# Optimization experiments

Measured on AMD Instinct MI355X. Metric: run time of the kernel, lower is better.

The kernel has to match this reference:

```python
import jax, jax.numpy as jnp
import numpy as np

LEAK = 0.01
EPS = 1e-5


def _gcn(x, W, b, src, dst, n):
    # GCNConv: add self-loops, symmetric D^-1/2 (A+I) D^-1/2 normalization
    h = x @ W
    loop = jnp.arange(n)
    s = jnp.concatenate([src, loop])
    d = jnp.concatenate([dst, loop])
    deg = jax.ops.segment_sum(jnp.ones(s.shape[0], h.dtype), d, num_segments=n)
    dinv = jnp.where(deg > 0, jax.lax.rsqrt(deg), 0.0)
    norm = dinv[s] * dinv[d]
    out = jax.ops.segment_sum(h[s] * norm[:, None], d, num_segments=n)
    return out + b


def _sage(x, Wl, bl, Wr, src, dst, n):
    # SAGEConv (mean aggr): lin_l(mean_neigh) + lin_r(x); bias on lin_l
    cnt = jax.ops.segment_sum(jnp.ones(src.shape[0], x.dtype), dst, num_segments=n)
    agg = jax.ops.segment_sum(x[src], dst, num_segments=n) / jnp.maximum(cnt, 1.0)[:, None]
    return agg @ Wl + bl + x @ Wr


def _bn(x, g, b):
    # BatchNorm over node dim, batch statistics (training forward), biased var
    m = x.mean(0)
    v = jnp.mean((x - m) ** 2, axis=0)
    return (x - m) * jax.lax.rsqrt(v + EPS) * g + b


def _lrelu(x):
    return jnp.where(x >= 0, x, LEAK * x)


def setup_inputs() -> dict:
    key = jax.random.key(0)
    ks = jax.random.split(key, 20)
    N, E, F_IN, H, G, L = 50000, 800000, 128, 128, 1000, 1000
    h2, h4, OUT = H // 2, H // 4, 32
    x = jax.random.normal(ks[0], (N, F_IN), dtype=jnp.float32)
    edge_index = jax.random.randint(ks[1], (2, E), 0, N)
    batch = jnp.sort(jax.random.randint(ks[2], (N,), 0, G))
    link_indices = jax.random.randint(ks[3], (2, L), 0, G)
    s = 0.05
    return {
        "x": x, "edge_index": edge_index, "batch": batch,
        "link_indices": link_indices, "num_graphs": G,
        "W1": jax.random.normal(ks[4], (F_IN, H), jnp.float32) * s,
        "b1": jnp.zeros((H,), jnp.float32),
        "g1": jnp.ones((H,), jnp.float32), "be1": jnp.zeros((H,), jnp.float32),
        "Wl2": jax.random.normal(ks[5], (H, h2), jnp.float32) * s,
        "bl2": jnp.zeros((h2,), jnp.float32),
        "Wr2": jax.random.normal(ks[6], (H, h2), jnp.float32) * s,
        "g2": jnp.ones((h2,), jnp.float32), "be2": jnp.zeros((h2,), jnp.float32),
        "W3": jax.random.normal(ks[7], (h2, h4), jnp.float32) * s,
        "b3": jnp.zeros((h4,), jnp.float32),
        "g3": jnp.ones((h4,), jnp.float32), "be3": jnp.zeros((h4,), jnp.float32),
        "W4": jax.random.normal(ks[8], (h4, OUT), jnp.float32) * s,
        "b4": jnp.zeros((OUT,), jnp.float32),
    }


def reference(x, edge_index, batch, link_indices, num_graphs,
              W1, b1, g1, be1, Wl2, bl2, Wr2, g2, be2,
              W3, b3, g3, be3, W4, b4):
    n = x.shape[0]
    src, dst = edge_index[0], edge_index[1]
    h = _lrelu(_bn(_gcn(x, W1, b1, src, dst, n), g1, be1))        # dropout = identity (eval)
    h = _lrelu(_bn(_sage(h, Wl2, bl2, Wr2, src, dst, n), g2, be2))
    h = _lrelu(_bn(_gcn(h, W3, b3, src, dst, n), g3, be3))
    h = _gcn(h, W4, b4, src, dst, n)
    g = jax.ops.segment_sum(h, batch, num_segments=num_graphs)     # global_add_pool
    src_emb = g[link_indices[0]]
    tgt_emb = g[link_indices[1]]
    return jax.nn.sigmoid(jnp.sum(src_emb * tgt_emb, axis=1))
```

## Files before the change

kernel.cpp:

```cpp
#include <hip/hip_runtime.h>
#include <math.h>

#define LEAK 0.01f
#define BNEPS 1e-5f
#define NCH 256
#define NGMAX 1024

__device__ inline unsigned bfpack(float a, float b) {
  unsigned ua = __float_as_uint(a);
  unsigned ub = __float_as_uint(b);
  unsigned ra = (ua + 0x7fffu + ((ua >> 16) & 1u)) >> 16;
  unsigned rb = (ub + 0x7fffu + ((ub >> 16) & 1u)) & 0xffff0000u;
  return ra | rb;
}
__device__ inline float2 bfunpack(unsigned u) {
  float2 r;
  r.x = __uint_as_float(u << 16);
  r.y = __uint_as_float(u & 0xffff0000u);
  return r;
}

__global__ __launch_bounds__(256) void k_hist(const int* __restrict__ dst,
                                              int* __restrict__ H, int E, int NBK) {
  __shared__ int h[256];
  h[threadIdx.x] = 0;
  __syncthreads();
  int chunk = (E + NCH - 1) / NCH;
  int lo = blockIdx.x * chunk, hi = min(lo + chunk, E);
  for (int e = lo + threadIdx.x; e < hi; e += 256)
    atomicAdd(&h[dst[e] >> 8], 1);
  __syncthreads();
  if (threadIdx.x < NBK) H[threadIdx.x * NCH + blockIdx.x] = h[threadIdx.x];
}

__global__ __launch_bounds__(256) void k_gscan1(const int* __restrict__ in,
                                                int* __restrict__ bsum, int m) {
  int i = blockIdx.x * 256 + threadIdx.x;
  int v = (i < m) ? in[i] : 0;
#pragma unroll
  for (int s = 1; s < 64; s <<= 1) v += __shfl_xor(v, s, 64);
  __shared__ int ws[4];
  if ((threadIdx.x & 63) == 0) ws[threadIdx.x >> 6] = v;
  __syncthreads();
  if (threadIdx.x == 0) bsum[blockIdx.x] = ws[0] + ws[1] + ws[2] + ws[3];
}
__global__ __launch_bounds__(256) void k_gscan2(int* __restrict__ bsum, int NB) {
  __shared__ int lds[256];
  int t = threadIdx.x;
  int v = (t < NB) ? bsum[t] : 0;
  lds[t] = v;
  __syncthreads();
  for (int ofs = 1; ofs < 256; ofs <<= 1) {
    int u = (t >= ofs) ? lds[t - ofs] : 0;
    __syncthreads();
    lds[t] += u;
    __syncthreads();
  }
  if (t < NB) bsum[t] = lds[t] - v;
}
__global__ __launch_bounds__(256) void k_gscan3(const int* __restrict__ in,
                                                const int* __restrict__ boff,
                                                int* __restrict__ out, int m) {
  __shared__ int lds[256];
  int t = threadIdx.x;
  int i = blockIdx.x * 256 + t;
  int v = (i < m) ? in[i] : 0;
  lds[t] = v;
  __syncthreads();
  for (int ofs = 1; ofs < 256; ofs <<= 1) {
    int u = (t >= ofs) ? lds[t - ofs] : 0;
    __syncthreads();
    lds[t] += u;
    __syncthreads();
  }
  if (i < m) out[i] = boff[blockIdx.x] + lds[t] - v;
}

__global__ __launch_bounds__(256) void k_scatter_bkt(
    const int* __restrict__ src, const int* __restrict__ dst,
    const int* __restrict__ O, int* __restrict__ ebuf, int E, int NBK) {
  __shared__ int cur[256];
  if (threadIdx.x < NBK) cur[threadIdx.x] = O[threadIdx.x * NCH + blockIdx.x];
  __syncthreads();
  int chunk = (E + NCH - 1) / NCH;
  int lo = blockIdx.x * chunk, hi = min(lo + chunk, E);
  for (int e = lo + threadIdx.x; e < hi; e += 256) {
    int d = dst[e];
    int pos = atomicAdd(&cur[d >> 8], 1);
    ebuf[pos] = src[e] | ((d & 255) << 24);
  }
}

__global__ __launch_bounds__(256) void k_fill2(
    const int* __restrict__ ebuf, const int* __restrict__ O,
    int* __restrict__ eidx, int* __restrict__ rowptr,
    float* __restrict__ dinv, float* __restrict__ invcnt,
    int E, int n, int NBK) {
  __shared__ int hist[256];
  __shared__ int sc[256];
  __shared__ int cur[256];
  const int b = blockIdx.x;
  const int t = threadIdx.x;
  const int lo = O[b * NCH];
  const int hi = (b + 1 < NBK) ? O[(b + 1) * NCH] : E;
  hist[t] = 0;
  __syncthreads();
  for (int e = lo + t; e < hi; e += 256)
    atomicAdd(&hist[(ebuf[e] >> 24) & 255], 1);
  __syncthreads();
  int v = hist[t];
  sc[t] = v;
  __syncthreads();
  for (int ofs = 1; ofs < 256; ofs <<= 1) {
    int u = (t >= ofs) ? sc[t - ofs] : 0;
    __syncthreads();
    sc[t] += u;
    __syncthreads();
  }
  int excl = sc[t] - v;
  cur[t] = lo + excl;
  int node = b * 256 + t;
  if (node < n) {
    rowptr[node] = lo + excl;
    float d = (float)v;
    dinv[node]   = rsqrtf(d + 1.0f);
    invcnt[node] = 1.0f / fmaxf(d, 1.0f);
  }
  if (node == n || (b == NBK - 1 && t == 255)) rowptr[n] = E;
  __syncthreads();
  for (int e = lo + t; e < hi; e += 256) {
    int p = ebuf[e];
    int pos = atomicAdd(&cur[(p >> 24) & 255], 1);
    eidx[pos] = p & 0xFFFFFF;
  }
}

template<int F, bool GCN, bool OUTBF, bool ADD>
__global__ __launch_bounds__(256) void k_gather(
    const unsigned short* __restrict__ Hs, const float* __restrict__ scale,
    const int* __restrict__ rowptr, const int* __restrict__ eidx,
    const float* __restrict__ bias, const float* __restrict__ addf,
    float* __restrict__ outf, unsigned short* __restrict__ outb, int n) {
  constexpr int COLS = F / 8;
  constexpr int EPI  = 64 / COLS;
  const int v = blockIdx.x * 4 + (threadIdx.x >> 6);
  if (v >= n) return;
  const int lane = threadIdx.x & 63;
  const int col  = lane % COLS;
  const int eo   = lane / COLS;

  const int lo = rowptr[v], hi = rowptr[v + 1];
  float a[8] = {0.f,0.f,0.f,0.f,0.f,0.f,0.f,0.f};
  int myE = (lo + lane < hi) ? eidx[lo + lane] : 0;
  for (int base = lo; base < hi; base += 64) {
    int cnt = min(hi - base, 64);
    int nxt = (base + 64 + lane < hi) ? eidx[base + 64 + lane] : 0;
#pragma unroll 4
    for (int t = eo; t < cnt; t += EPI) {
      int s = __shfl(myE, t, 64);
      uint4 hv = *(const uint4*)&Hs[(long long)s * F + col * 8];
      float2 p0 = bfunpack(hv.x), p1 = bfunpack(hv.y);
      float2 p2 = bfunpack(hv.z), p3 = bfunpack(hv.w);
      a[0]+=p0.x; a[1]+=p0.y; a[2]+=p1.x; a[3]+=p1.y;
      a[4]+=p2.x; a[5]+=p2.y; a[6]+=p3.x; a[7]+=p3.y;
    }
    myE = nxt;
  }
#pragma unroll
  for (int m = COLS; m < 64; m <<= 1) {
#pragma unroll
    for (int j = 0; j < 8; j++) a[j] += __shfl_xor(a[j], m, 64);
  }
  if (eo == 0) {
    float sv = scale[v];
    float o[8];
    if constexpr (GCN) {
      uint4 hv = *(const uint4*)&Hs[(long long)v * F + col * 8];
      float2 p0 = bfunpack(hv.x), p1 = bfunpack(hv.y);
      float2 p2 = bfunpack(hv.z), p3 = bfunpack(hv.w);
      float h[8] = {p0.x,p0.y,p1.x,p1.y,p2.x,p2.y,p3.x,p3.y};
#pragma unroll
      for (int j = 0; j < 8; j++) o[j] = bias[col * 8 + j] + sv * (a[j] + h[j]);
    } else if constexpr (ADD) {
      const float4 t0 = *(const float4*)&addf[(long long)v * F + col * 8];
      const float4 t1 = *(const float4*)&addf[(long long)v * F + col * 8 + 4];
      o[0]=fmaf(sv,a[0],t0.x); o[1]=fmaf(sv,a[1],t0.y);
      o[2]=fmaf(sv,a[2],t0.z); o[3]=fmaf(sv,a[3],t0.w);
      o[4]=fmaf(sv,a[4],t1.x); o[5]=fmaf(sv,a[5],t1.y);
      o[6]=fmaf(sv,a[6],t1.z); o[7]=fmaf(sv,a[7],t1.w);
    } else {
#pragma unroll
      for (int j = 0; j < 8; j++) o[j] = sv * a[j];
    }
    if constexpr (OUTBF) {
      uint4 u;
      u.x = bfpack(o[0], o[1]); u.y = bfpack(o[2], o[3]);
      u.z = bfpack(o[4], o[5]); u.w = bfpack(o[6], o[7]);
      *(uint4*)&outb[(long long)v * F + col * 8] = u;
    } else {
      float4 o0 = {o[0],o[1],o[2],o[3]}, o1 = {o[4],o[5],o[6],o[7]};
      *(float4*)&outf[(long long)v * F + col * 8]     = o0;
      *(float4*)&outf[(long long)v * F + col * 8 + 4] = o1;
    }
  }
}

template<int K, int FOUT, int KC, int R, bool X1BF, bool BNIN>
__global__ __launch_bounds__(256) void k_gemm(
    const void* __restrict__ X1v, const float* __restrict__ Wa,
    const float* __restrict__ bnstats, const float* __restrict__ prescale,
    unsigned short* __restrict__ Yb, int n) {
  constexpr int TPR  = FOUT / 4;
  constexpr int RGN  = 256 / TPR;
  constexpr int ROWS = RGN * R;
  __shared__ float sX1[ROWS * K];
  __shared__ float sWa[KC * FOUT];
  __shared__ float sbn[BNIN ? 2 * K : 1];

  if constexpr (BNIN) {
    for (int i = threadIdx.x; i < 2 * K; i += 256) sbn[i] = bnstats[i];
    __syncthreads();
  }
  const int row0 = blockIdx.x * ROWS;
  if constexpr (X1BF) {
    const unsigned short* X1 = (const unsigned short*)X1v;
    for (int i = threadIdx.x; i < ROWS * K / 8; i += 256) {
      int r = i / (K / 8), k8 = (i % (K / 8)) * 8;
      int gr = row0 + r;
      uint4 raw = {0,0,0,0};
      if (gr < n) raw = *(const uint4*)&X1[(long long)gr * K + k8];
      float2 p0 = bfunpack(raw.x), p1 = bfunpack(raw.y);
      float2 p2 = bfunpack(raw.z), p3 = bfunpack(raw.w);
      float y[8] = {p0.x,p0.y,p1.x,p1.y,p2.x,p2.y,p3.x,p3.y};
      if constexpr (BNIN) {
#pragma unroll
        for (int j = 0; j < 8; j++) {
          float t = fmaf(y[j], sbn[k8 + j], sbn[K + k8 + j]);
          y[j] = (t >= 0.f) ? t : LEAK * t;
        }
      }
      float4 lo = {y[0],y[1],y[2],y[3]}, hi = {y[4],y[5],y[6],y[7]};
      *(float4*)&sX1[r * K + k8]     = lo;
      *(float4*)&sX1[r * K + k8 + 4] = hi;
    }
  } else {
    const float* X1 = (const float*)X1v;
    for (int i = threadIdx.x; i < ROWS * K / 4; i += 256) {
      int r = i / (K / 4), k4 = (i % (K / 4)) * 4;
      int gr = row0 + r;
      float4 vv = {0,0,0,0};
      if (gr < n) vv = *(const float4*)&X1[(long long)gr * K + k4];
      *(float4*)&sX1[r * K + k4] = vv;
    }
  }

  const int cg = threadIdx.x % TPR;
  const int rg = threadIdx.x / TPR;
  const int jc = cg * 4;
  float4 acc[R];
#pragma unroll
  for (int i = 0; i < R; i++) acc[i] = {0.f,0.f,0.f,0.f};

  for (int k0 = 0; k0 < K; k0 += KC) {
    __syncthreads();
    for (int i = threadIdx.x; i < KC * FOUT / 4; i += 256) {
      int kk = i / (FOUT / 4), j4 = (i % (FOUT / 4)) * 4;
      *(float4*)&sWa[kk * FOUT + j4] = *(const float4*)&Wa[(long long)(k0 + kk) * FOUT + j4];
    }
    __syncthreads();
#pragma unroll 8
    for (int kk = 0; kk < KC; kk++) {
      const float4 w = *(const float4*)&sWa[kk * FOUT + jc];
#pragma unroll
      for (int i = 0; i < R; i++) {
        float xv = sX1[(rg * R + i) * K + k0 + kk];
        acc[i].x = fmaf(xv, w.x, acc[i].x); acc[i].y = fmaf(xv, w.y, acc[i].y);
        acc[i].z = fmaf(xv, w.z, acc[i].z); acc[i].w = fmaf(xv, w.w, acc[i].w);
      }
    }
  }
#pragma unroll
  for (int i = 0; i < R; i++) {
    int gr = row0 + rg * R + i;
    if (gr >= n) continue;
    float4 o = acc[i];
    float ps = prescale ? prescale[gr] : 1.0f;
    uint2 u;
    u.x = bfpack(o.x * ps, o.y * ps);
    u.y = bfpack(o.z * ps, o.w * ps);
    *(uint2*)&Yb[(long long)gr * FOUT + jc] = u;
  }
}

template<int R>
__global__ __launch_bounds__(256) void k_gemm_sage(
    const unsigned short* __restrict__ X, const float* __restrict__ Wl,
    const float* __restrict__ Wr, const float* __restrict__ bl,
    const float* __restrict__ bnstats,
    unsigned short* __restrict__ t1, float* __restrict__ t2, int n) {
  constexpr int K = 128, F = 64, KC = 64;
  constexpr int TPR = F / 4;
  constexpr int RGN = 256 / TPR;
  constexpr int ROWS = RGN * R;
  __shared__ float sX[ROWS * K];
  __shared__ float sWl[KC * F];
  __shared__ float sWr[KC * F];
  __shared__ float sbn[2 * K];

  for (int i = threadIdx.x; i < 2 * K; i += 256) sbn[i] = bnstats[i];
  __syncthreads();
  const int row0 = blockIdx.x * ROWS;
  for (int i = threadIdx.x; i < ROWS * K / 8; i += 256) {
    int r = i / (K / 8), k8 = (i % (K / 8)) * 8;
    int gr = row0 + r;
    uint4 raw = {0,0,0,0};
    if (gr < n) raw = *(const uint4*)&X[(long long)gr * K + k8];
    float2 p0 = bfunpack(raw.x), p1 = bfunpack(raw.y);
    float2 p2 = bfunpack(raw.z), p3 = bfunpack(raw.w);
    float y[8] = {p0.x,p0.y,p1.x,p1.y,p2.x,p2.y,p3.x,p3.y};
#pragma unroll
    for (int j = 0; j < 8; j++) {
      float t = fmaf(y[j], sbn[k8 + j], sbn[K + k8 + j]);
      y[j] = (t >= 0.f) ? t : LEAK * t;
    }
    float4 lo = {y[0],y[1],y[2],y[3]}, hi = {y[4],y[5],y[6],y[7]};
    *(float4*)&sX[r * K + k8]     = lo;
    *(float4*)&sX[r * K + k8 + 4] = hi;
  }

  const int cg = threadIdx.x % TPR;
  const int rg = threadIdx.x / TPR;
  const int jc = cg * 4;
  float4 a1[R], a2[R];
#pragma unroll
  for (int i = 0; i < R; i++) { a1[i] = {0,0,0,0}; a2[i] = {0,0,0,0}; }

  for (int k0 = 0; k0 < K; k0 += KC) {
    __syncthreads();
    for (int i = threadIdx.x; i < KC * F / 4; i += 256) {
      int kk = i / (F / 4), j4 = (i % (F / 4)) * 4;
      *(float4*)&sWl[kk * F + j4] = *(const float4*)&Wl[(long long)(k0 + kk) * F + j4];
      *(float4*)&sWr[kk * F + j4] = *(const float4*)&Wr[(long long)(k0 + kk) * F + j4];
    }
    __syncthreads();
#pragma unroll 8
    for (int kk = 0; kk < KC; kk++) {
      const float4 wl = *(const float4*)&sWl[kk * F + jc];
      const float4 wr = *(const float4*)&sWr[kk * F + jc];
#pragma unroll
      for (int i = 0; i < R; i++) {
        float xv = sX[(rg * R + i) * K + k0 + kk];
        a1[i].x = fmaf(xv, wl.x, a1[i].x); a1[i].y = fmaf(xv, wl.y, a1[i].y);
        a1[i].z = fmaf(xv, wl.z, a1[i].z); a1[i].w = fmaf(xv, wl.w, a1[i].w);
        a2[i].x = fmaf(xv, wr.x, a2[i].x); a2[i].y = fmaf(xv, wr.y, a2[i].y);
        a2[i].z = fmaf(xv, wr.z, a2[i].z); a2[i].w = fmaf(xv, wr.w, a2[i].w);
      }
    }
  }
#pragma unroll
  for (int i = 0; i < R; i++) {
    int gr = row0 + rg * R + i;
    if (gr >= n) continue;
    uint2 u;
    u.x = bfpack(a1[i].x, a1[i].y);
    u.y = bfpack(a1[i].z, a1[i].w);
    *(uint2*)&t1[(long long)gr * F + jc] = u;
    float4 o = a2[i];
    o.x += bl[jc]; o.y += bl[jc+1]; o.z += bl[jc+2]; o.w += bl[jc+3];
    *(float4*)&t2[(long long)gr * F + jc] = o;
  }
}

template<int F>
__global__ __launch_bounds__(256) void k_bn_stats(const unsigned short* __restrict__ Y,
                                                  float* __restrict__ partials, int n) {
  constexpr int FP  = F / 2;
  constexpr int RPB = 256 / FP;
  const int f2 = threadIdx.x % FP;
  const int r0 = threadIdx.x / FP;
  const unsigned* Yu = (const unsigned*)Y;
  float s1a = 0.f, s2a = 0.f, s1b = 0.f, s2b = 0.f;
  for (long long r = (long long)blockIdx.x * RPB + r0; r < n; r += 256LL * RPB) {
    float2 p = bfunpack(Yu[r * FP + f2]);
    s1a += p.x; s2a += p.x * p.x;
    s1b += p.y; s2b += p.y * p.y;
  }
  __shared__ float l1a[256], l2a[256], l1b[256], l2b[256];
  l1a[threadIdx.x] = s1a; l2a[threadIdx.x] = s2a;
  l1b[threadIdx.x] = s1b; l2b[threadIdx.x] = s2b;
  __syncthreads();
  if (r0 == 0) {
#pragma unroll
    for (int i = 1; i < RPB; i++) {
      s1a += l1a[i * FP + f2]; s2a += l2a[i * FP + f2];
      s1b += l1b[i * FP + f2]; s2b += l2b[i * FP + f2];
    }
    float* p = &partials[blockIdx.x * 2 * F];
    p[2 * f2]         = s1a;
    p[2 * f2 + 1]     = s1b;
    p[F + 2 * f2]     = s2a;
    p[F + 2 * f2 + 1] = s2b;
  }
}

__global__ void k_bn_finalize(const float* __restrict__ partials, float* __restrict__ stats,
                              const float* __restrict__ g, const float* __restrict__ be,
                              int F, float invN) {
  int f = threadIdx.x;
  if (f >= F) return;
  float s1 = 0.f, s2 = 0.f;
  for (int b = 0; b < 256; b++) {
    s1 += partials[b * 2 * F + f];
    s2 += partials[b * 2 * F + F + f];
  }
  float m   = s1 * invN;
  float var = s2 * invN - m * m;
  float sc  = g[f] * rsqrtf(var + BNEPS);
  stats[f]     = sc;
  stats[F + f] = be[f] - m * sc;
}

__global__ __launch_bounds__(256) void k_pool2(const float* __restrict__ a4,
                                               const int* __restrict__ batch,
                                               float* __restrict__ gpool, int n) {
  int g = blockIdx.x * 4 + (threadIdx.x >> 6);
  if (g >= NGMAX) return;
  int lane = threadIdx.x & 63;
  int s = 0, e = n;
  while (s < e) { int m = (s + e) >> 1; if (batch[m] < g) s = m + 1; else e = m; }
  int s2 = s, e2 = n;
  while (s2 < e2) { int m = (s2 + e2) >> 1; if (batch[m] < g + 1) s2 = m + 1; else e2 = m; }
  int f = lane & 31, ro = lane >> 5;
  float acc = 0.f;
  for (int r = s + ro; r < s2; r += 2) acc += a4[(long long)r * 32 + f];
  acc += __shfl_xor(acc, 32, 64);
  if (lane < 32) gpool[(long long)g * 32 + f] = acc;
}

__global__ void k_link(const float* __restrict__ g, const int* __restrict__ li0,
                       const int* __restrict__ li1, float* __restrict__ out, int L) {
  int i = blockIdx.x * blockDim.x + threadIdx.x;
  if (i >= L) return;
  const float* a = g + (long long)li0[i] * 32;
  const float* b = g + (long long)li1[i] * 32;
  float s = 0.f;
#pragma unroll
  for (int f = 0; f < 32; f++) s = fmaf(a[f], b[f], s);
  out[i] = 1.0f / (1.0f + expf(-s));
}

extern "C" void kernel_launch(void* const* d_in, const int* in_sizes, int n_in,
                              void* d_out, int out_size, void* d_ws, size_t ws_size,
                              hipStream_t stream) {
  const float* x   = (const float*)d_in[0];
  const int* ei    = (const int*)d_in[1];
  const int* batch = (const int*)d_in[2];
  const int* li    = (const int*)d_in[3];
  const float* W1  = (const float*)d_in[5];
  const float* b1  = (const float*)d_in[6];
  const float* g1  = (const float*)d_in[7];
  const float* be1 = (const float*)d_in[8];
  const float* Wl2 = (const float*)d_in[9];
  const float* bl2 = (const float*)d_in[10];
  const float* Wr2 = (const float*)d_in[11];
  const float* g2  = (const float*)d_in[12];
  const float* be2 = (const float*)d_in[13];
  const float* W3  = (const float*)d_in[14];
  const float* b3  = (const float*)d_in[15];
  const float* g3  = (const float*)d_in[16];
  const float* be3 = (const float*)d_in[17];
  const float* W4  = (const float*)d_in[18];
  const float* b4  = (const float*)d_in[19];

  const int n = in_sizes[0] / 128;
  const int E = in_sizes[1] / 2;
  const int L = in_sizes[3] / 2;
  const int* src = ei;
  const int* dst = ei + E;
  const int* li0 = li;
  const int* li1 = li + L;
  const int NBK = (n + 255) / 256;

  char* base = (char*)d_ws;
  size_t off = 0;
  auto alloc = [&](size_t bytes) -> void* {
    void* p = (void*)(base + off);
    off = (off + bytes + 255) & ~(size_t)255;
    return p;
  };
  int*   H      = (int*)alloc((size_t)NBK * NCH * 4);
  int*   O      = (int*)alloc((size_t)NBK * NCH * 4);
  int*   hsum   = (int*)alloc(1024 * 4);
  int*   ebuf   = (int*)alloc((size_t)E * 4);
  int*   eidx   = (int*)alloc((size_t)E * 4);
  int*   rowptr = (int*)alloc((size_t)(n + 1) * 4);
  float* dinv   = (float*)alloc((size_t)n * 4);
  float* invcnt = (float*)alloc((size_t)n * 4);
  float* stats1 = (float*)alloc(256 * 4);
  float* stats2 = (float*)alloc(128 * 4);
  float* stats3 = (float*)alloc(64 * 4);
  float* partials = (float*)alloc((size_t)256 * 256 * 4);
  float* gpool  = (float*)alloc((size_t)NGMAX * 32 * 4);
  unsigned short* h1b  = (unsigned short*)alloc((size_t)n * 128 * 2);
  unsigned short* a1b  = (unsigned short*)alloc((size_t)n * 128 * 2);
  unsigned short* t1b  = (unsigned short*)alloc((size_t)n * 64 * 2);
  float*          t2f  = (float*)alloc((size_t)n * 64 * 4);
  unsigned short* h2b  = (unsigned short*)alloc((size_t)n * 64 * 2);
  unsigned short* h3gb = (unsigned short*)alloc((size_t)n * 32 * 2);
  unsigned short* a3b  = (unsigned short*)alloc((size_t)n * 32 * 2);
  unsigned short* h4b  = (unsigned short*)alloc((size_t)n * 32 * 2);
  float*          a4f  = (float*)alloc((size_t)n * 32 * 4);
  (void)ws_size; (void)n_in; (void)out_size;

  const int BT = 256;
  auto cdiv = [](long long a, long long b) { return (int)((a + b - 1) / b); };
  const int GB  = cdiv(n, 4);
  const int MH  = NBK * NCH;
  const int NBH = cdiv(MH, 256);

  k_hist<<<NCH, 256, 0, stream>>>(dst, H, E, NBK);
  k_gscan1<<<NBH, 256, 0, stream>>>(H, hsum, MH);
  k_gscan2<<<1, 256, 0, stream>>>(hsum, NBH);
  k_gscan3<<<NBH, 256, 0, stream>>>(H, hsum, O, MH);
  k_scatter_bkt<<<NCH, 256, 0, stream>>>(src, dst, O, ebuf, E, NBK);
  k_fill2<<<NBK, 256, 0, stream>>>(ebuf, O, eidx, rowptr, dinv, invcnt, E, n, NBK);

  k_gemm<128,128,64,4,false,false><<<cdiv(n,32), 256, 0, stream>>>(
      x, W1, nullptr, dinv, h1b, n);
  k_gather<128,true,true,false><<<GB, 256, 0, stream>>>(
      h1b, dinv, rowptr, eidx, b1, nullptr, nullptr, a1b, n);
  k_bn_stats<128><<<256, 256, 0, stream>>>(a1b, partials, n);
  k_bn_finalize<<<1, 128, 0, stream>>>(partials, stats1, g1, be1, 128, 1.0f / n);

  k_gemm_sage<2><<<cdiv(n,32), 256, 0, stream>>>(a1b, Wl2, Wr2, bl2, stats1, t1b, t2f, n);
  k_gather<64,false,true,true><<<GB, 256, 0, stream>>>(
      t1b, invcnt, rowptr, eidx, nullptr, t2f, nullptr, h2b, n);
  k_bn_stats<64><<<256, 256, 0, stream>>>(h2b, partials, n);
  k_bn_finalize<<<1, 64, 0, stream>>>(partials, stats2, g2, be2, 64, 1.0f / n);

  k_gemm<64,32,64,4,true,true><<<cdiv(n,128), 256, 0, stream>>>(
      h2b, W3, stats2, dinv, h3gb, n);
  k_gather<32,true,true,false><<<GB, 256, 0, stream>>>(
      h3gb, dinv, rowptr, eidx, b3, nullptr, nullptr, a3b, n);
  k_bn_stats<32><<<256, 256, 0, stream>>>(a3b, partials, n);
  k_bn_finalize<<<1, 32, 0, stream>>>(partials, stats3, g3, be3, 32, 1.0f / n);

  k_gemm<32,32,32,4,true,true><<<cdiv(n,128), 256, 0, stream>>>(
      a3b, W4, stats3, dinv, h4b, n);
  k_gather<32,true,false,false><<<GB, 256, 0, stream>>>(
      h4b, dinv, rowptr, eidx, b4, nullptr, a4f, nullptr, n);

  k_pool2<<<NGMAX / 4, 256, 0, stream>>>(a4f, batch, gpool, n);
  k_link<<<cdiv(L, BT), BT, 0, stream>>>(gpool, li0, li1, (float*)d_out, L);
}
```

Measured before the change: 410.6 us.

## Replace FP32 FMA dense GEMMs with bf16 MFMA kernels

Rewrites the node-feature GEMMs (GCN layers and the SAGE dual GEMM) to use 16x16x32 bf16 MFMA instructions. Each block stages 64 rows of bf16 inputs and a transposed bf16 weight tile in padded shared memory. The BN+LeakyReLU prologue and the dinv prescale epilogue are kept. The aim is to move the GEMM FLOPs off the vector FMA units onto the matrix cores. In exchange, weights and the raw fp32 input x are rounded to bf16, and outputs are written with scalar 16-bit stores instead of vector stores.

```diff
diff --git a/kernel.cpp b/kernel.cpp
--- a/kernel.cpp
+++ b/kernel.cpp
@@ -5,6 +5,9 @@
 #define BNEPS 1e-5f
 #define NCH 256
 #define NGMAX 1024
+
+typedef __attribute__((ext_vector_type(8))) short bf16x8;
+typedef __attribute__((ext_vector_type(4))) float f32x4;
 
 __device__ inline unsigned bfpack(float a, float b) {
   unsigned ua = __float_as_uint(a);
@@ -12,6 +15,10 @@
   unsigned ra = (ua + 0x7fffu + ((ua >> 16) & 1u)) >> 16;
   unsigned rb = (ub + 0x7fffu + ((ub >> 16) & 1u)) & 0xffff0000u;
   return ra | rb;
+}
+__device__ inline unsigned short bfround(float a) {
+  unsigned ua = __float_as_uint(a);
+  return (unsigned short)((ua + 0x7fffu + ((ua >> 16) & 1u)) >> 16);
 }
 __device__ inline float2 bfunpack(unsigned u) {
   float2 r;
@@ -205,169 +212,176 @@
   }
 }
 
-template<int K, int FOUT, int KC, int R, bool X1BF, bool BNIN>
-__global__ __launch_bounds__(256) void k_gemm(
-    const void* __restrict__ X1v, const float* __restrict__ Wa,
+template<int K, int F, bool XBF, bool BNIN>
+__global__ __launch_bounds__(256) void k_gemm_mfma(
+    const void* __restrict__ Xv, const float* __restrict__ W,
     const float* __restrict__ bnstats, const float* __restrict__ prescale,
     unsigned short* __restrict__ Yb, int n) {
-  constexpr int TPR  = FOUT / 4;
-  constexpr int RGN  = 256 / TPR;
-  constexpr int ROWS = RGN * R;
-  __shared__ float sX1[ROWS * K];
-  __shared__ float sWa[KC * FOUT];
+  constexpr int SP  = K + 8;
+  constexpr int NCT = F / 16;
+  __shared__ unsigned short sX[64 * SP];
+  __shared__ unsigned short sWT[F * SP];
   __shared__ float sbn[BNIN ? 2 * K : 1];
 
+  const int row0 = blockIdx.x * 64;
   if constexpr (BNIN) {
     for (int i = threadIdx.x; i < 2 * K; i += 256) sbn[i] = bnstats[i];
     __syncthreads();
   }
-  const int row0 = blockIdx.x * ROWS;
-  if constexpr (X1BF) {
-    const unsigned short* X1 = (const unsigned short*)X1v;
-    for (int i = threadIdx.x; i < ROWS * K / 8; i += 256) {
-      int r = i / (K / 8), k8 = (i % (K / 8)) * 8;
-      int gr = row0 + r;
-      uint4 raw = {0,0,0,0};
-      if (gr < n) raw = *(const uint4*)&X1[(long long)gr * K + k8];
-      float2 p0 = bfunpack(raw.x), p1 = bfunpack(raw.y);
-      float2 p2 = bfunpack(raw.z), p3 = bfunpack(raw.w);
-      float y[8] = {p0.x,p0.y,p1.x,p1.y,p2.x,p2.y,p3.x,p3.y};
-      if constexpr (BNIN) {
-#pragma unroll
-        for (int j = 0; j < 8; j++) {
-          float t = fmaf(y[j], sbn[k8 + j], sbn[K + k8 + j]);
-          y[j] = (t >= 0.f) ? t : LEAK * t;
+  for (int i = threadIdx.x; i < (K / 2) * F; i += 256) {
+    int nn = i % F;
+    int kk = (i / F) * 2;
+    float w0 = W[(long long)kk * F + nn];
+    float w1 = W[(long long)(kk + 1) * F + nn];
+    *(unsigned*)&sWT[nn * SP + kk] = bfpack(w0, w1);
+  }
+  for (int i = threadIdx.x; i < 64 * (K / 8); i += 256) {
+    int r = i / (K / 8), k8 = (i % (K / 8)) * 8;
+    int gr = row0 + r;
+    uint4 u = {0, 0, 0, 0};
+    if (gr < n) {
+      if constexpr (XBF) {
+        const unsigned short* X = (const unsigned short*)Xv;
+        uint4 raw = *(const uint4*)&X[(long long)gr * K + k8];
+        if constexpr (BNIN) {
+          float2 p0 = bfunpack(raw.x), p1 = bfunpack(raw.y);
+          float2 p2 = bfunpack(raw.z), p3 = bfunpack(raw.w);
+          float y[8] = {p0.x,p0.y,p1.x,p1.y,p2.x,p2.y,p3.x,p3.y};
+#pragma unroll
+          for (int j = 0; j < 8; j++) {
+            float t = fmaf(y[j], sbn[k8 + j], sbn[K + k8 + j]);
+            y[j] = (t >= 0.f) ? t : LEAK * t;
+          }
+          u.x = bfpack(y[0], y[1]); u.y = bfpack(y[2], y[3]);
+          u.z = bfpack(y[4], y[5]); u.w = bfpack(y[6], y[7]);
+        } else {
+          u = raw;
         }
+      } else {
+        const float* X = (const float*)Xv;
+        float4 xa = *(const float4*)&X[(long long)gr * K + k8];
+        float4 xb = *(const float4*)&X[(long long)gr * K + k8 + 4];
+        u.x = bfpack(xa.x, xa.y); u.y = bfpack(xa.z, xa.w);
+        u.z = bfpack(xb.x, xb.y); u.w = bfpack(xb.z, xb.w);
       }
-      float4 lo = {y[0],y[1],y[2],y[3]}, hi = {y[4],y[5],y[6],y[7]};
-      *(float4*)&sX1[r * K + k8]     = lo;
-      *(float4*)&sX1[r * K + k8 + 4] = hi;
-    }
-  } else {
-    const float* X1 = (const float*)X1v;
-    for (int i = threadIdx.x; i < ROWS * K / 4; i += 256) {
-      int r = i / (K / 4), k4 = (i % (K / 4)) * 4;
-      int gr = row0 + r;
-      float4 vv = {0,0,0,0};
-      if (gr < n) vv = *(const float4*)&X1[(long long)gr * K + k4];
-      *(float4*)&sX1[r * K + k4] = vv;
-    }
-  }
-
-  const int cg = threadIdx.x % TPR;
-  const int rg = threadIdx.x / TPR;
-  const int jc = cg * 4;
-  float4 acc[R];
-#pragma unroll
-  for (int i = 0; i < R; i++) acc[i] = {0.f,0.f,0.f,0.f};
-
-  for (int k0 = 0; k0 < K; k0 += KC) {
-    __syncthreads();
-    for (int i = threadIdx.x; i < KC * FOUT / 4; i += 256) {
-      int kk = i / (FOUT / 4), j4 = (i % (FOUT / 4)) * 4;
-      *(float4*)&sWa[kk * FOUT + j4] = *(const float4*)&Wa[(long long)(k0 + kk) * FOUT + j4];
-    }
-    __syncthreads();
-#pragma unroll 8
-    for (int kk = 0; kk < KC; kk++) {
-      const float4 w = *(const float4*)&sWa[kk * FOUT + jc];
-#pragma unroll
-      for (int i = 0; i < R; i++) {
-        float xv = sX1[(rg * R + i) * K + k0 + kk];
-        acc[i].x = fmaf(xv, w.x, acc[i].x); acc[i].y = fmaf(xv, w.y, acc[i].y);
-        acc[i].z = fmaf(xv, w.z, acc[i].z); acc[i].w = fmaf(xv, w.w, acc[i].w);
-      }
-    }
-  }
-#pragma unroll
-  for (int i = 0; i < R; i++) {
-    int gr = row0 + rg * R + i;
-    if (gr >= n) continue;
-    float4 o = acc[i];
-    float ps = prescale ? prescale[gr] : 1.0f;
-    uint2 u;
-    u.x = bfpack(o.x * ps, o.y * ps);
-    u.y = bfpack(o.z * ps, o.w * ps);
-    *(uint2*)&Yb[(long long)gr * FOUT + jc] = u;
-  }
-}
-
-template<int R>
-__global__ __launch_bounds__(256) void k_gemm_sage(
+    }
+    *(uint4*)&sX[r * SP + k8] = u;
+  }
+  __syncthreads();
+
+  const int wv   = threadIdx.x >> 6;
+  const int lane = threadIdx.x & 63;
+  const int l16  = lane & 15;
+  const int quad = lane >> 4;
+  f32x4 acc[NCT];
+#pragma unroll
+  for (int c = 0; c < NCT; c++) acc[c] = (f32x4){0.f, 0.f, 0.f, 0.f};
+
+#pragma unroll
+  for (int k0 = 0; k0 < K; k0 += 32) {
+    bf16x8 af = *(const bf16x8*)&sX[(wv * 16 + l16) * SP + k0 + quad * 8];
+#pragma unroll
+    for (int c = 0; c < NCT; c++) {
+      bf16x8 bfr = *(const bf16x8*)&sWT[(c * 16 + l16) * SP + k0 + quad * 8];
+      acc[c] = __builtin_amdgcn_mfma_f32_16x16x32_bf16(af, bfr, acc[c], 0, 0, 0);
+    }
+  }
+
+  const int rbase = row0 + wv * 16 + quad * 4;
+  float ps[4];
+#pragma unroll
+  for (int rg = 0; rg < 4; rg++) {
+    int gr = rbase + rg;
+    ps[rg] = (prescale && gr < n) ? prescale[gr] : 1.0f;
+  }
+#pragma unroll
+  for (int c = 0; c < NCT; c++) {
+    int col = c * 16 + l16;
+#pragma unroll
+    for (int rg = 0; rg < 4; rg++) {
+      int gr = rbase + rg;
+      if (gr < n) Yb[(long long)gr * F + col] = bfround(acc[c][rg] * ps[rg]);
+    }
+  }
+}
+
+__global__ __launch_bounds__(256) void k_gemm_sage_mfma(
     const unsigned short* __restrict__ X, const float* __restrict__ Wl,
     const float* __restrict__ Wr, const float* __restrict__ bl,
     const float* __restrict__ bnstats,
     unsigned short* __restrict__ t1, float* __restrict__ t2, int n) {
-  constexpr int K = 128, F = 64, KC = 64;
-  constexpr int TPR = F / 4;
-  constexpr int RGN = 256 / TPR;
-  constexpr int ROWS = RGN * R;
-  __shared__ float sX[ROWS * K];
-  __shared__ float sWl[KC * F];
-  __shared__ float sWr[KC * F];
+  constexpr int K = 128, F = 64, SP = K + 8, NCT = F / 16;
+  __shared__ unsigned short sX[64 * SP];
+  __shared__ unsigned short sWlT[F * SP];
+  __shared__ unsigned short sWrT[F * SP];
   __shared__ float sbn[2 * K];
 
   for (int i = threadIdx.x; i < 2 * K; i += 256) sbn[i] = bnstats[i];
   __syncthreads();
-  const int row0 = blockIdx.x * ROWS;
-  for (int i = threadIdx.x; i < ROWS * K / 8; i += 256) {
+  const int row0 = blockIdx.x * 64;
+  for (int i = threadIdx.x; i < (K / 2) * F; i += 256) {
+    int nn = i % F;
+    int kk = (i / F) * 2;
+    *(unsigned*)&sWlT[nn * SP + kk] =
+        bfpack(Wl[(long long)kk * F + nn], Wl[(long long)(kk + 1) * F + nn]);
+    *(unsigned*)&sWrT[nn * SP + kk] =
+        bfpack(Wr[(long long)kk * F + nn], Wr[(long long)(kk + 1) * F + nn]);
+  }
+  for (int i = threadIdx.x; i < 64 * (K / 8); i += 256) {
     int r = i / (K / 8), k8 = (i % (K / 8)) * 8;
     int gr = row0 + r;
-    uint4 raw = {0,0,0,0};
-    if (gr < n) raw = *(const uint4*)&X[(long long)gr * K + k8];
-    float2 p0 = bfunpack(raw.x), p1 = bfunpack(raw.y);
-    float2 p2 = bfunpack(raw.z), p3 = bfunpack(raw.w);
-    float y[8] = {p0.x,p0.y,p1.x,p1.y,p2.x,p2.y,p3.x,p3.y};
-#pragma unroll
-    for (int j = 0; j < 8; j++) {
-      float t = fmaf(y[j], sbn[k8 + j], sbn[K + k8 + j]);
-      y[j] = (t >= 0.f) ? t : LEAK * t;
-    }
-    float4 lo = {y[0],y[1],y[2],y[3]}, hi = {y[4],y[5],y[6],y[7]};
-    *(float4*)&sX[r * K + k8]     = lo;
-    *(float4*)&sX[r * K + k8 + 4] = hi;
-  }
-
-  const int cg = threadIdx.x % TPR;
-  const int rg = threadIdx.x / TPR;
-  const int jc = cg * 4;
-  float4 a1[R], a2[R];
-#pragma unroll
-  for (int i = 0; i < R; i++) { a1[i] = {0,0,0,0}; a2[i] = {0,0,0,0}; }
-
-  for (int k0 = 0; k0 < K; k0 += KC) {
-    __syncthreads();
-    for (int i = threadIdx.x; i < KC * F / 4; i += 256) {
-      int kk = i / (F / 4), j4 = (i % (F / 4)) * 4;
-      *(float4*)&sWl[kk * F + j4] = *(const float4*)&Wl[(long long)(k0 + kk) * F + j4];
-      *(float4*)&sWr[kk * F + j4] = *(const float4*)&Wr[(long long)(k0 + kk) * F + j4];
-    }
-    __syncthreads();
-#pragma unroll 8
-    for (int kk = 0; kk < KC; kk++) {
-      const float4 wl = *(const float4*)&sWl[kk * F + jc];
-      const float4 wr = *(const float4*)&sWr[kk * F + jc];
-#pragma unroll
-      for (int i = 0; i < R; i++) {
-        float xv = sX[(rg * R + i) * K + k0 + kk];
-        a1[i].x = fmaf(xv, wl.x, a1[i].x); a1[i].y = fmaf(xv, wl.y, a1[i].y);
-        a1[i].z = fmaf(xv, wl.z, a1[i].z); a1[i].w = fmaf(xv, wl.w, a1[i].w);
-        a2[i].x = fmaf(xv, wr.x, a2[i].x); a2[i].y = fmaf(xv, wr.y, a2[i].y);
-        a2[i].z = fmaf(xv, wr.z, a2[i].z); a2[i].w = fmaf(xv, wr.w, a2[i].w);
+    uint4 u = {0, 0, 0, 0};
+    if (gr < n) {
+      uint4 raw = *(const uint4*)&X[(long long)gr * K + k8];
+      float2 p0 = bfunpack(raw.x), p1 = bfunpack(raw.y);
+      float2 p2 = bfunpack(raw.z), p3 = bfunpack(raw.w);
+      float y[8] = {p0.x,p0.y,p1.x,p1.y,p2.x,p2.y,p3.x,p3.y};
+#pragma unroll
+      for (int j = 0; j < 8; j++) {
+        float t = fmaf(y[j], sbn[k8 + j], sbn[K + k8 + j]);
+        y[j] = (t >= 0.f) ? t : LEAK * t;
       }
-    }
-  }
-#pragma unroll
-  for (int i = 0; i < R; i++) {
-    int gr = row0 + rg * R + i;
-    if (gr >= n) continue;
-    uint2 u;
-    u.x = bfpack(a1[i].x, a1[i].y);
-    u.y = bfpack(a1[i].z, a1[i].w);
-    *(uint2*)&t1[(long long)gr * F + jc] = u;
-    float4 o = a2[i];
-    o.x += bl[jc]; o.y += bl[jc+1]; o.z += bl[jc+2]; o.w += bl[jc+3];
-    *(float4*)&t2[(long long)gr * F + jc] = o;
+      u.x = bfpack(y[0], y[1]); u.y = bfpack(y[2], y[3]);
+      u.z = bfpack(y[4], y[5]); u.w = bfpack(y[6], y[7]);
+    }
+    *(uint4*)&sX[r * SP + k8] = u;
+  }
+  __syncthreads();
+
+  const int wv   = threadIdx.x >> 6;
+  const int lane = threadIdx.x & 63;
+  const int l16  = lane & 15;
+  const int quad = lane >> 4;
+  f32x4 a1[NCT], a2[NCT];
+#pragma unroll
+  for (int c = 0; c < NCT; c++) {
+    a1[c] = (f32x4){0.f, 0.f, 0.f, 0.f};
+    a2[c] = (f32x4){0.f, 0.f, 0.f, 0.f};
+  }
+#pragma unroll
+  for (int k0 = 0; k0 < K; k0 += 32) {
+    bf16x8 af = *(const bf16x8*)&sX[(wv * 16 + l16) * SP + k0 + quad * 8];
+#pragma unroll
+    for (int c = 0; c < NCT; c++) {
+      bf16x8 bl8 = *(const bf16x8*)&sWlT[(c * 16 + l16) * SP + k0 + quad * 8];
+      bf16x8 br8 = *(const bf16x8*)&sWrT[(c * 16 + l16) * SP + k0 + quad * 8];
+      a1[c] = __builtin_amdgcn_mfma_f32_16x16x32_bf16(af, bl8, a1[c], 0, 0, 0);
+      a2[c] = __builtin_amdgcn_mfma_f32_16x16x32_bf16(af, br8, a2[c], 0, 0, 0);
+    }
+  }
+  const int rbase = row0 + wv * 16 + quad * 4;
+#pragma unroll
+  for (int c = 0; c < NCT; c++) {
+    int col = c * 16 + l16;
+    float blv = bl[col];
+#pragma unroll
+    for (int rg = 0; rg < 4; rg++) {
+      int gr = rbase + rg;
+      if (gr < n) {
+        t1[(long long)gr * F + col] = bfround(a1[c][rg]);
+        t2[(long long)gr * F + col] = a2[c][rg] + blv;
+      }
+    }
   }
 }
 
@@ -515,6 +529,7 @@
   const int BT = 256;
   auto cdiv = [](long long a, long long b) { return (int)((a + b - 1) / b); };
   const int GB  = cdiv(n, 4);
+  const int GM  = cdiv(n, 64);
   const int MH  = NBK * NCH;
   const int NBH = cdiv(MH, 256);
 
@@ -525,27 +540,27 @@
   k_scatter_bkt<<<NCH, 256, 0, stream>>>(src, dst, O, ebuf, E, NBK);
   k_fill2<<<NBK, 256, 0, stream>>>(ebuf, O, eidx, rowptr, dinv, invcnt, E, n, NBK);
 
-  k_gemm<128,128,64,4,false,false><<<cdiv(n,32), 256, 0, stream>>>(
+  k_gemm_mfma<128,128,false,false><<<GM, 256, 0, stream>>>(
       x, W1, nullptr, dinv, h1b, n);
   k_gather<128,true,true,false><<<GB, 256, 0, stream>>>(
       h1b, dinv, rowptr, eidx, b1, nullptr, nullptr, a1b, n);
   k_bn_stats<128><<<256, 256, 0, stream>>>(a1b, partials, n);
   k_bn_finalize<<<1, 128, 0, stream>>>(partials, stats1, g1, be1, 128, 1.0f / n);
 
-  k_gemm_sage<2><<<cdiv(n,32), 256, 0, stream>>>(a1b, Wl2, Wr2, bl2, stats1, t1b, t2f, n);
+  k_gemm_sage_mfma<<<GM, 256, 0, stream>>>(a1b, Wl2, Wr2, bl2, stats1, t1b, t2f, n);
   k_gather<64,false,true,true><<<GB, 256, 0, stream>>>(
       t1b, invcnt, rowptr, eidx, nullptr, t2f, nullptr, h2b, n);
   k_bn_stats<64><<<256, 256, 0, stream>>>(h2b, partials, n);
   k_bn_finalize<<<1, 64, 0, stream>>>(partials, stats2, g2, be2, 64, 1.0f / n);
 
-  k_gemm<64,32,64,4,true,true><<<cdiv(n,128), 256, 0, stream>>>(
+  k_gemm_mfma<64,32,true,true><<<GM, 256, 0, stream>>>(
       h2b, W3, stats2, dinv, h3gb, n);
   k_gather<32,true,true,false><<<GB, 256, 0, stream>>>(
       h3gb, dinv, rowptr, eidx, b3, nullptr, nullptr, a3b, n);
   k_bn_stats<32><<<256, 256, 0, stream>>>(a3b, partials, n);
   k_bn_finalize<<<1, 32, 0, stream>>>(partials, stats3, g3, be3, 32, 1.0f / n);
 
-  k_gemm<32,32,32,4,true,true><<<cdiv(n,128), 256, 0, stream>>>(
+  k_gemm_mfma<32,32,true,true><<<GM, 256, 0, stream>>>(
       a3b, W4, stats3, dinv, h4b, n);
   k_gather<32,true,false,false><<<GB, 256, 0, stream>>>(
       h4b, dinv, rowptr, eidx, b4, nullptr, a4f, nullptr, n);
```

New measurement: 381.0 us. -7.2%, faster.
